# Kernel tuning notes

Hardware: AMD Instinct MI355X
Metric: run time of the kernel (lower is better)

The kernel has to match this reference:

```python
import jax, jax.numpy as jnp
import numpy as np

B, S, D, H = 4, 2048, 1024, 16
DK = D // H


def setup_inputs() -> dict:
    key = jax.random.key(0)
    ks = jax.random.split(key, 9)
    sc = 1.0 / np.sqrt(D)
    return {
        "query": jax.random.normal(ks[0], (B, S, D), jnp.float32),
        "key": jax.random.normal(ks[1], (B, S, D), jnp.float32),
        "value": jax.random.normal(ks[2], (B, S, D), jnp.float32),
        "Wq": jax.random.normal(ks[3], (D, D), jnp.float32) * sc,
        "bq": jax.random.normal(ks[4], (D,), jnp.float32) * sc,
        "Wk": jax.random.normal(ks[5], (D, D), jnp.float32) * sc,
        "bk": jax.random.normal(ks[6], (D,), jnp.float32) * sc,
        "Wv": jax.random.normal(ks[7], (D, D), jnp.float32) * sc,
        "bv": jax.random.normal(ks[8], (D,), jnp.float32) * sc,
    }


def reference(query, key, value, Wq, bq, Wk, bk, Wv, bv):
    # QKV projections, split into heads: [B,S,D] -> [B,H,S,DK]
    q = (query @ Wq + bq).reshape(B, S, H, DK).transpose(0, 2, 1, 3)
    k = (key @ Wk + bk).reshape(B, S, H, DK).transpose(0, 2, 1, 3)
    v = (value @ Wv + bv).reshape(B, S, H, DK).transpose(0, 2, 1, 3)
    # NOTE: original module applies NO 1/sqrt(d_k) scaling
    attn = jnp.einsum("bhqd,bhkd->bhqk", q, k)
    attn = jax.nn.softmax(attn, axis=-1)  # dropout is identity at inference
    ctx = jnp.einsum("bhqk,bhkd->bhqd", attn, v)
    ctx = ctx.transpose(0, 2, 1, 3).reshape(B, S, D)
    # original adds residual to raw concatenated context (no output projection)
    return ctx + query
```

## Files before the change

kernel.cpp:

```cpp
#include <hip/hip_runtime.h>
#include <hip/hip_bf16.h>
#include <stdint.h>

#define Bb 4
#define Ss 2048
#define Dd 1024
#define Hh 16
#define DK 64
#define BH 64
#define Mm 8192
#define KVT 64

typedef __attribute__((ext_vector_type(8))) _Float16 f16x8;
typedef __attribute__((ext_vector_type(4))) _Float16 f16x4;
typedef __attribute__((ext_vector_type(2))) __fp16 fp16x2;
typedef __attribute__((ext_vector_type(4))) float f32x4;
typedef __attribute__((ext_vector_type(16))) float f32x16;
typedef __attribute__((ext_vector_type(2))) unsigned uint2v;

__device__ __forceinline__ void gload16(const _Float16* g, _Float16* lds) {
  __builtin_amdgcn_global_load_lds((const __attribute__((address_space(1))) unsigned int*)g,
                                   (__attribute__((address_space(3))) unsigned int*)lds, 16, 0, 0);
}

#if __has_builtin(__builtin_amdgcn_exp2f)
__device__ __forceinline__ float ex2(float x) { return __builtin_amdgcn_exp2f(x); }
#else
__device__ __forceinline__ float ex2(float x) {
  float r; asm("v_exp_f32 %0, %1" : "=v"(r) : "v"(x)); return r;
}
#endif

__device__ __forceinline__ unsigned pk2u(float a, float b) {
  union { fp16x2 h; unsigned u; } x;
  x.h = __builtin_amdgcn_cvt_pkrtz(a, b);
  return x.u;
}

__global__ __launch_bounds__(256) void cvt_act(const float* __restrict__ q,
                                               const float* __restrict__ k,
                                               const float* __restrict__ v,
                                               _Float16* __restrict__ xq,
                                               _Float16* __restrict__ xk,
                                               _Float16* __restrict__ xv) {
  const float* src = blockIdx.z == 0 ? q : (blockIdx.z == 1 ? k : v);
  _Float16* dst = blockIdx.z == 0 ? xq : (blockIdx.z == 1 ? xk : xv);
  int i = (blockIdx.x * 256 + threadIdx.x) * 8;
  float4 a = *(const float4*)(src + i);
  float4 b = *(const float4*)(src + i + 4);
  union { f16x8 v8; _Float16 h[8]; } o;
  o.h[0] = (_Float16)a.x; o.h[1] = (_Float16)a.y; o.h[2] = (_Float16)a.z; o.h[3] = (_Float16)a.w;
  o.h[4] = (_Float16)b.x; o.h[5] = (_Float16)b.y; o.h[6] = (_Float16)b.z; o.h[7] = (_Float16)b.w;
  *(f16x8*)(dst + i) = o.v8;
}

__global__ __launch_bounds__(256) void cvt_wt(const float* __restrict__ wq,
                                              const float* __restrict__ wk,
                                              const float* __restrict__ wv,
                                              _Float16* __restrict__ tq,
                                              _Float16* __restrict__ tk,
                                              _Float16* __restrict__ tv) {
  const float* w = blockIdx.z == 0 ? wq : (blockIdx.z == 1 ? wk : wv);
  _Float16* o = blockIdx.z == 0 ? tq : (blockIdx.z == 1 ? tk : tv);
  float wscale = blockIdx.z == 0 ? 1.4426950408889634f : 1.0f;
  __shared__ float tile[64][65];
  int k0 = blockIdx.x * 64;
  int n0 = blockIdx.y * 64;
  int t = threadIdx.x;
  int tr = t >> 4;
  int tc = (t & 15) * 4;
  for (int i = 0; i < 4; i++) {
    int r = i * 16 + tr;
    float4 val = *(const float4*)(w + (k0 + r) * Dd + n0 + tc);
    tile[r][tc + 0] = val.x; tile[r][tc + 1] = val.y;
    tile[r][tc + 2] = val.z; tile[r][tc + 3] = val.w;
  }
  __syncthreads();
  for (int i = 0; i < 2; i++) {
    int vdx = t + 256 * i;
    int rn = vdx >> 3;
    int c8 = (vdx & 7) * 8;
    union { f16x8 v8; _Float16 h[8]; } o2;
    for (int j = 0; j < 8; j++) o2.h[j] = (_Float16)(tile[c8 + j][rn] * wscale);
    *(f16x8*)(o + (n0 + rn) * Dd + k0 + c8) = o2.v8;
  }
}

__global__ __launch_bounds__(256) void gemm_qkv(
    const _Float16* __restrict__ xq, const _Float16* __restrict__ xk,
    const _Float16* __restrict__ xv,
    const _Float16* __restrict__ wtq, const _Float16* __restrict__ wtk,
    const _Float16* __restrict__ wtv,
    const float* __restrict__ bq, const float* __restrict__ bk, const float* __restrict__ bv,
    _Float16* __restrict__ oq, _Float16* __restrict__ ok,
    _Float16* __restrict__ ov) {
  int z = blockIdx.z;
  const _Float16* A  = z == 0 ? xq  : (z == 1 ? xk  : xv);
  const _Float16* Bt = z == 0 ? wtq : (z == 1 ? wtk : wtv);
  const float* bias  = z == 0 ? bq  : (z == 1 ? bk  : bv);
  _Float16* out      = z == 0 ? oq  : (z == 1 ? ok  : ov);
  float bscale       = z == 0 ? 1.4426950408889634f : 1.0f;

  __shared__ _Float16 As[128 * 64];
  __shared__ _Float16 Bs[128 * 64];

  int tid = threadIdx.x;
  int w = tid >> 6;
  int l = tid & 63;
  int lr = l & 15, lk = l >> 4;
  int m0 = blockIdx.x * 128;
  int n0 = blockIdx.y * 128;
  int wr = (w >> 1) * 64;
  int wc = (w & 1) * 64;

  f32x4 acc[4][4] = {};

  for (int kt = 0; kt < Dd; kt += 64) {
    __syncthreads();
    for (int i = 0; i < 4; i++) {
      int fbase = i * 256 + w * 64;
      int f = fbase + l;
      int r = f >> 3, c = (f & 7) * 8;
      gload16(A + (m0 + r) * Dd + kt + c, &As[fbase * 8]);
      gload16(Bt + (n0 + r) * Dd + kt + c, &Bs[fbase * 8]);
    }
    __syncthreads();
    for (int kh = 0; kh < 2; kh++) {
      f16x8 af[4], bfr[4];
      for (int mi = 0; mi < 4; mi++)
        af[mi] = *(const f16x8*)&As[(wr + mi * 16 + lr) * 64 + kh * 32 + lk * 8];
      for (int ni = 0; ni < 4; ni++)
        bfr[ni] = *(const f16x8*)&Bs[(wc + ni * 16 + lr) * 64 + kh * 32 + lk * 8];
      for (int mi = 0; mi < 4; mi++)
        for (int ni = 0; ni < 4; ni++)
          acc[mi][ni] = __builtin_amdgcn_mfma_f32_16x16x32_f16(af[mi], bfr[ni], acc[mi][ni], 0, 0, 0);
    }
  }

  if (z == 2) {
    for (int mi = 0; mi < 4; mi++) {
      for (int ni = 0; ni < 4; ni++) {
        int n = n0 + wc + ni * 16 + lr;
        float bval = bias[n];
        int h = n >> 6, dk = n & 63;
        int m = m0 + wr + mi * 16 + lk * 4;
        int b = m >> 11, s = m & 2047;
        f16x4 o4;
        for (int j = 0; j < 4; j++) o4[j] = (_Float16)(acc[mi][ni][j] + bval);
        *(f16x4*)(out + ((size_t)((b * Hh + h) * DK + dk) * Ss + s)) = o4;
      }
    }
  } else {
    for (int mi = 0; mi < 4; mi++) {
      for (int ni = 0; ni < 4; ni++) {
        int n = n0 + wc + ni * 16 + lr;
        float bval = bias[n] * bscale;
        int h = n >> 6, dk = n & 63;
        for (int j = 0; j < 4; j++) {
          int m = m0 + wr + mi * 16 + lk * 4 + j;
          int b = m >> 11, s = m & 2047;
          out[((b * Hh + h) * Ss + s) * DK + dk] = (_Float16)(acc[mi][ni][j] + bval);
        }
      }
    }
  }
}

__global__ __launch_bounds__(256) void attn(const _Float16* __restrict__ Qb,
                                            const _Float16* __restrict__ Kb,
                                            const _Float16* __restrict__ Vt,
                                            const float* __restrict__ query,
                                            float* __restrict__ outp) {
  __shared__ _Float16 Kl[2][KVT * 64];
  __shared__ _Float16 Vl[2][KVT * 64];

  int tid = threadIdx.x;
  int w = tid >> 6, l = tid & 63;
  int l31 = l & 31, hi = l >> 5;
  int bh = blockIdx.x;
  int q0 = blockIdx.y * 128 + w * 32;
  const _Float16* Qp = Qb + bh * (Ss * DK);
  const _Float16* Kp = Kb + bh * (Ss * DK);
  const _Float16* Vp = Vt + bh * (DK * Ss);

  int srow = l >> 3;
  int sslot = (l & 7) ^ (srow & 7);
  int w16 = w * 16;
  const _Float16* ksrc0 = Kp + (w16 + srow) * DK + sslot * 8;
  const _Float16* ksrc1 = Kp + (w16 + 8 + srow) * DK + sslot * 8;
  const _Float16* vsrc0 = Vp + (w16 + srow) * Ss + sslot * 8;
  const _Float16* vsrc1 = Vp + (w16 + 8 + srow) * Ss + sslot * 8;

#define STAGE(KV0, BUF)                                                   \
  {                                                                       \
    gload16(ksrc0 + (KV0) * DK, &Kl[BUF][w16 * 64]);                      \
    gload16(ksrc1 + (KV0) * DK, &Kl[BUF][(w16 + 8) * 64]);                \
    gload16(vsrc0 + (KV0), &Vl[BUF][w16 * 64]);                           \
    gload16(vsrc1 + (KV0), &Vl[BUF][(w16 + 8) * 64]);                     \
  }

  f16x8 qf[4];
#pragma unroll
  for (int s = 0; s < 4; s++)
    qf[s] = *(const f16x8*)(Qp + (q0 + l31) * DK + s * 16 + hi * 8);

  f32x16 o0 = {}, o1 = {};
  float mrun = -1e30f, lrun = 0.f;

  int kv7 = l31 & 7;
  int rslot[4];
#pragma unroll
  for (int s = 0; s < 4; s++) rslot[s] = ((s * 2 + hi) ^ kv7) * 8;

  STAGE(0, 0)
  __syncthreads();

  int cur = 0;
  for (int kv0 = 0; kv0 < Ss; kv0 += KVT) {
    if (kv0 + KVT < Ss) STAGE(kv0 + KVT, cur ^ 1)

    const _Float16* Kc = &Kl[cur][0];
    f32x16 s0 = {}, s1 = {};
#pragma unroll
    for (int s = 0; s < 4; s++) {
      f16x8 ka = *(const f16x8*)&Kc[l31 * 64 + rslot[s]];
      s0 = __builtin_amdgcn_mfma_f32_32x32x16_f16(ka, qf[s], s0, 0, 0, 0);
    }
#pragma unroll
    for (int s = 0; s < 4; s++) {
      f16x8 kb = *(const f16x8*)&Kc[(32 + l31) * 64 + rslot[s]];
      s1 = __builtin_amdgcn_mfma_f32_32x32x16_f16(kb, qf[s], s1, 0, 0, 0);
    }

    float m8[8];
#pragma unroll
    for (int r = 0; r < 8; r++)
      m8[r] = fmaxf(fmaxf(s0[r], s0[r + 8]), fmaxf(s1[r], s1[r + 8]));
#pragma unroll
    for (int d = 4; d >= 1; d >>= 1)
#pragma unroll
      for (int r = 0; r < 4; r++) if (r < d) m8[r] = fmaxf(m8[r], m8[r + d]);
    float pm = fmaxf(m8[0], __shfl_xor(m8[0], 32));

    if (!__all(pm - mrun <= 8.f)) {
      float mn = fmaxf(mrun, pm);
      float sc_ = ex2(mrun - mn);
      mrun = mn;
      lrun *= sc_;
#pragma unroll
      for (int r = 0; r < 16; r++) { o0[r] *= sc_; o1[r] *= sc_; }
    }
#pragma unroll
    for (int r = 0; r < 16; r++) {
      s0[r] = ex2(s0[r] - mrun);
      s1[r] = ex2(s1[r] - mrun);
    }
    float s8[8];
#pragma unroll
    for (int r = 0; r < 8; r++) s8[r] = (s0[r] + s0[r + 8]) + (s1[r] + s1[r + 8]);
#pragma unroll
    for (int d = 4; d >= 1; d >>= 1)
#pragma unroll
      for (int r = 0; r < 4; r++) if (r < d) s8[r] += s8[r + d];
    lrun += s8[0];

    const _Float16* Vc = &Vl[cur][0];
#define PVSTEP(SRC, OFF, KST)                                                   \
    {                                                                           \
      unsigned a0 = pk2u(SRC[(OFF) + 0], SRC[(OFF) + 1]);                       \
      unsigned a1 = pk2u(SRC[(OFF) + 2], SRC[(OFF) + 3]);                       \
      unsigned b0 = pk2u(SRC[(OFF) + 4], SRC[(OFF) + 5]);                       \
      unsigned b1 = pk2u(SRC[(OFF) + 6], SRC[(OFF) + 7]);                       \
      uint2v r0 = __builtin_amdgcn_permlane32_swap(a0, b0, false, false);       \
      uint2v r1 = __builtin_amdgcn_permlane32_swap(a1, b1, false, false);       \
      union { unsigned u[4]; f16x8 v; } pf;                                     \
      pf.u[0] = r0[0]; pf.u[1] = r1[0]; pf.u[2] = r0[1]; pf.u[3] = r1[1];       \
      f16x8 v0 = *(const f16x8*)&Vc[l31 * 64 + rslot[KST]];                     \
      f16x8 v1 = *(const f16x8*)&Vc[(32 + l31) * 64 + rslot[KST]];              \
      o0 = __builtin_amdgcn_mfma_f32_32x32x16_f16(v0, pf.v, o0, 0, 0, 0);       \
      o1 = __builtin_amdgcn_mfma_f32_32x32x16_f16(v1, pf.v, o1, 0, 0, 0);       \
    }
    PVSTEP(s0, 0, 0)
    PVSTEP(s0, 8, 1)
    PVSTEP(s1, 0, 2)
    PVSTEP(s1, 8, 3)
#undef PVSTEP

    __syncthreads();
    cur ^= 1;
  }

  lrun += __shfl_xor(lrun, 32);
  int b = bh >> 4, h = bh & 15;
  float inv = 1.f / lrun;
  int base = (b * Ss + q0 + l31) * Dd + h * 64;
#pragma unroll
  for (int rq = 0; rq < 4; rq++) {
    int d0 = rq * 8 + hi * 4;
    float4 qv0 = *(const float4*)(query + base + d0);
    float4 ov0;
    ov0.x = o0[rq * 4 + 0] * inv + qv0.x;
    ov0.y = o0[rq * 4 + 1] * inv + qv0.y;
    ov0.z = o0[rq * 4 + 2] * inv + qv0.z;
    ov0.w = o0[rq * 4 + 3] * inv + qv0.w;
    *(float4*)(outp + base + d0) = ov0;
    float4 qv1 = *(const float4*)(query + base + 32 + d0);
    float4 ov1;
    ov1.x = o1[rq * 4 + 0] * inv + qv1.x;
    ov1.y = o1[rq * 4 + 1] * inv + qv1.y;
    ov1.z = o1[rq * 4 + 2] * inv + qv1.z;
    ov1.w = o1[rq * 4 + 3] * inv + qv1.w;
    *(float4*)(outp + base + 32 + d0) = ov1;
  }
#undef STAGE
}

extern "C" void kernel_launch(void* const* d_in, const int* in_sizes, int n_in,
                              void* d_out, int out_size, void* d_ws, size_t ws_size,
                              hipStream_t stream) {
  const float* query = (const float*)d_in[0];
  const float* key   = (const float*)d_in[1];
  const float* value = (const float*)d_in[2];
  const float* Wq = (const float*)d_in[3];
  const float* bq = (const float*)d_in[4];
  const float* Wk = (const float*)d_in[5];
  const float* bk = (const float*)d_in[6];
  const float* Wv = (const float*)d_in[7];
  const float* bv = (const float*)d_in[8];
  float* out = (float*)d_out;

  _Float16* ws = (_Float16*)d_ws;
  const size_t ACT = (size_t)Mm * Dd;
  const size_t WSZ = (size_t)Dd * Dd;
  _Float16* Xq   = ws;
  _Float16* Xk   = Xq + ACT;
  _Float16* Xv   = Xk + ACT;
  _Float16* Wtq  = Xv + ACT;
  _Float16* Wtk  = Wtq + WSZ;
  _Float16* Wtv  = Wtk + WSZ;
  _Float16* Qb   = Wtv + WSZ;
  _Float16* Kb   = Qb + ACT;
  _Float16* VtT  = Kb + ACT;

  cvt_act<<<dim3(4096, 1, 3), dim3(256), 0, stream>>>(query, key, value, Xq, Xk, Xv);
  cvt_wt<<<dim3(16, 16, 3), dim3(256), 0, stream>>>(Wq, Wk, Wv, Wtq, Wtk, Wtv);
  gemm_qkv<<<dim3(64, 8, 3), dim3(256), 0, stream>>>(Xq, Xk, Xv, Wtq, Wtk, Wtv,
                                                     bq, bk, bv, Qb, Kb, VtT);
  attn<<<dim3(64, 16), dim3(256), 0, stream>>>(Qb, Kb, VtT, query, out);
}
```

Measured before the change: 221.2 us.

## Process 64 query rows per wave and compute row sums via MFMA

Each wave now handles two 32-row query tiles against the same K/V shared-memory tiles, doubling reuse of each LDS load and halving the grid to 512 blocks. The per-row softmax denominator is no longer reduced with scalar adds; it is accumulated by an extra MFMA against a ones vector alongside the PV product. This raises register pressure (four output accumulators plus two sum accumulators) and halves block count, which may reduce occupancy on a 256-CU device.

```diff
diff --git a/kernel.cpp b/kernel.cpp
--- a/kernel.cpp
+++ b/kernel.cpp
@@ -178,7 +178,7 @@
   int w = tid >> 6, l = tid & 63;
   int l31 = l & 31, hi = l >> 5;
   int bh = blockIdx.x;
-  int q0 = blockIdx.y * 128 + w * 32;
+  int q0 = blockIdx.y * 256 + w * 64;
   const _Float16* Qp = Qb + bh * (Ss * DK);
   const _Float16* Kp = Kb + bh * (Ss * DK);
   const _Float16* Vp = Vt + bh * (DK * Ss);
@@ -199,13 +199,20 @@
     gload16(vsrc1 + (KV0), &Vl[BUF][(w16 + 8) * 64]);                     \
   }
 
-  f16x8 qf[4];
+  f16x8 qfA[4], qfB[4];
 #pragma unroll
-  for (int s = 0; s < 4; s++)
-    qf[s] = *(const f16x8*)(Qp + (q0 + l31) * DK + s * 16 + hi * 8);
-
-  f32x16 o0 = {}, o1 = {};
-  float mrun = -1e30f, lrun = 0.f;
+  for (int s = 0; s < 4; s++) {
+    qfA[s] = *(const f16x8*)(Qp + (q0 + l31) * DK + s * 16 + hi * 8);
+    qfB[s] = *(const f16x8*)(Qp + (q0 + 32 + l31) * DK + s * 16 + hi * 8);
+  }
+
+  f16x8 ones;
+#pragma unroll
+  for (int j = 0; j < 8; j++) ones[j] = (_Float16)1.0f;
+
+  f32x16 oA0 = {}, oA1 = {}, oB0 = {}, oB1 = {};
+  f32x16 smA = {}, smB = {};
+  float mrunA = -1e30f, mrunB = -1e30f;
 
   int kv7 = l31 & 7;
   int rslot[4];
@@ -220,98 +227,111 @@
     if (kv0 + KVT < Ss) STAGE(kv0 + KVT, cur ^ 1)
 
     const _Float16* Kc = &Kl[cur][0];
-    f32x16 s0 = {}, s1 = {};
+    f32x16 sA0 = {}, sA1 = {}, sB0 = {}, sB1 = {};
 #pragma unroll
     for (int s = 0; s < 4; s++) {
       f16x8 ka = *(const f16x8*)&Kc[l31 * 64 + rslot[s]];
-      s0 = __builtin_amdgcn_mfma_f32_32x32x16_f16(ka, qf[s], s0, 0, 0, 0);
-    }
-#pragma unroll
-    for (int s = 0; s < 4; s++) {
       f16x8 kb = *(const f16x8*)&Kc[(32 + l31) * 64 + rslot[s]];
-      s1 = __builtin_amdgcn_mfma_f32_32x32x16_f16(kb, qf[s], s1, 0, 0, 0);
-    }
-
-    float m8[8];
-#pragma unroll
-    for (int r = 0; r < 8; r++)
-      m8[r] = fmaxf(fmaxf(s0[r], s0[r + 8]), fmaxf(s1[r], s1[r + 8]));
-#pragma unroll
-    for (int d = 4; d >= 1; d >>= 1)
-#pragma unroll
-      for (int r = 0; r < 4; r++) if (r < d) m8[r] = fmaxf(m8[r], m8[r + d]);
-    float pm = fmaxf(m8[0], __shfl_xor(m8[0], 32));
-
-    if (!__all(pm - mrun <= 8.f)) {
-      float mn = fmaxf(mrun, pm);
-      float sc_ = ex2(mrun - mn);
-      mrun = mn;
-      lrun *= sc_;
-#pragma unroll
-      for (int r = 0; r < 16; r++) { o0[r] *= sc_; o1[r] *= sc_; }
-    }
-#pragma unroll
-    for (int r = 0; r < 16; r++) {
-      s0[r] = ex2(s0[r] - mrun);
-      s1[r] = ex2(s1[r] - mrun);
-    }
-    float s8[8];
-#pragma unroll
-    for (int r = 0; r < 8; r++) s8[r] = (s0[r] + s0[r + 8]) + (s1[r] + s1[r + 8]);
-#pragma unroll
-    for (int d = 4; d >= 1; d >>= 1)
-#pragma unroll
-      for (int r = 0; r < 4; r++) if (r < d) s8[r] += s8[r + d];
-    lrun += s8[0];
+      sA0 = __builtin_amdgcn_mfma_f32_32x32x16_f16(ka, qfA[s], sA0, 0, 0, 0);
+      sA1 = __builtin_amdgcn_mfma_f32_32x32x16_f16(kb, qfA[s], sA1, 0, 0, 0);
+      sB0 = __builtin_amdgcn_mfma_f32_32x32x16_f16(ka, qfB[s], sB0, 0, 0, 0);
+      sB1 = __builtin_amdgcn_mfma_f32_32x32x16_f16(kb, qfB[s], sB1, 0, 0, 0);
+    }
+
+#define SOFTMAX(S0, S1, MRUN, O0, O1, SM)                                       \
+    {                                                                           \
+      float m8[8];                                                              \
+      _Pragma("unroll")                                                         \
+      for (int r = 0; r < 8; r++)                                               \
+        m8[r] = fmaxf(fmaxf(S0[r], S0[r + 8]), fmaxf(S1[r], S1[r + 8]));        \
+      _Pragma("unroll")                                                         \
+      for (int d = 4; d >= 1; d >>= 1)                                          \
+        for (int r = 0; r < 4; r++) if (r < d) m8[r] = fmaxf(m8[r], m8[r + d]); \
+      float pm = fmaxf(m8[0], __shfl_xor(m8[0], 32));                           \
+      if (!__all(pm - MRUN <= 8.f)) {                                           \
+        float mn = fmaxf(MRUN, pm);                                             \
+        float sc_ = ex2(MRUN - mn);                                             \
+        MRUN = mn;                                                              \
+        _Pragma("unroll")                                                       \
+        for (int r = 0; r < 16; r++) {                                          \
+          O0[r] *= sc_; O1[r] *= sc_; SM[r] *= sc_;                             \
+        }                                                                       \
+      }                                                                         \
+      _Pragma("unroll")                                                         \
+      for (int r = 0; r < 16; r++) {                                            \
+        S0[r] = ex2(S0[r] - MRUN);                                              \
+        S1[r] = ex2(S1[r] - MRUN);                                              \
+      }                                                                         \
+    }
+    SOFTMAX(sA0, sA1, mrunA, oA0, oA1, smA)
+    SOFTMAX(sB0, sB1, mrunB, oB0, oB1, smB)
+#undef SOFTMAX
 
     const _Float16* Vc = &Vl[cur][0];
-#define PVSTEP(SRC, OFF, KST)                                                   \
+#define PVSTEP(SA, SB, OFF, KST)                                                \
     {                                                                           \
-      unsigned a0 = pk2u(SRC[(OFF) + 0], SRC[(OFF) + 1]);                       \
-      unsigned a1 = pk2u(SRC[(OFF) + 2], SRC[(OFF) + 3]);                       \
-      unsigned b0 = pk2u(SRC[(OFF) + 4], SRC[(OFF) + 5]);                       \
-      unsigned b1 = pk2u(SRC[(OFF) + 6], SRC[(OFF) + 7]);                       \
-      uint2v r0 = __builtin_amdgcn_permlane32_swap(a0, b0, false, false);       \
-      uint2v r1 = __builtin_amdgcn_permlane32_swap(a1, b1, false, false);       \
-      union { unsigned u[4]; f16x8 v; } pf;                                     \
-      pf.u[0] = r0[0]; pf.u[1] = r1[0]; pf.u[2] = r0[1]; pf.u[3] = r1[1];       \
       f16x8 v0 = *(const f16x8*)&Vc[l31 * 64 + rslot[KST]];                     \
       f16x8 v1 = *(const f16x8*)&Vc[(32 + l31) * 64 + rslot[KST]];              \
-      o0 = __builtin_amdgcn_mfma_f32_32x32x16_f16(v0, pf.v, o0, 0, 0, 0);       \
-      o1 = __builtin_amdgcn_mfma_f32_32x32x16_f16(v1, pf.v, o1, 0, 0, 0);       \
-    }
-    PVSTEP(s0, 0, 0)
-    PVSTEP(s0, 8, 1)
-    PVSTEP(s1, 0, 2)
-    PVSTEP(s1, 8, 3)
+      unsigned aa0 = pk2u(SA[(OFF) + 0], SA[(OFF) + 1]);                        \
+      unsigned aa1 = pk2u(SA[(OFF) + 2], SA[(OFF) + 3]);                        \
+      unsigned ab0 = pk2u(SA[(OFF) + 4], SA[(OFF) + 5]);                        \
+      unsigned ab1 = pk2u(SA[(OFF) + 6], SA[(OFF) + 7]);                        \
+      uint2v ra0 = __builtin_amdgcn_permlane32_swap(aa0, ab0, false, false);    \
+      uint2v ra1 = __builtin_amdgcn_permlane32_swap(aa1, ab1, false, false);    \
+      union { unsigned u[4]; f16x8 v; } pfA;                                    \
+      pfA.u[0] = ra0[0]; pfA.u[1] = ra1[0]; pfA.u[2] = ra0[1]; pfA.u[3] = ra1[1];\
+      unsigned ba0 = pk2u(SB[(OFF) + 0], SB[(OFF) + 1]);                        \
+      unsigned ba1 = pk2u(SB[(OFF) + 2], SB[(OFF) + 3]);                        \
+      unsigned bb0 = pk2u(SB[(OFF) + 4], SB[(OFF) + 5]);                        \
+      unsigned bb1 = pk2u(SB[(OFF) + 6], SB[(OFF) + 7]);                        \
+      uint2v rb0 = __builtin_amdgcn_permlane32_swap(ba0, bb0, false, false);    \
+      uint2v rb1 = __builtin_amdgcn_permlane32_swap(ba1, bb1, false, false);    \
+      union { unsigned u[4]; f16x8 v; } pfB;                                    \
+      pfB.u[0] = rb0[0]; pfB.u[1] = rb1[0]; pfB.u[2] = rb0[1]; pfB.u[3] = rb1[1];\
+      oA0 = __builtin_amdgcn_mfma_f32_32x32x16_f16(v0, pfA.v, oA0, 0, 0, 0);    \
+      oA1 = __builtin_amdgcn_mfma_f32_32x32x16_f16(v1, pfA.v, oA1, 0, 0, 0);    \
+      oB0 = __builtin_amdgcn_mfma_f32_32x32x16_f16(v0, pfB.v, oB0, 0, 0, 0);    \
+      oB1 = __builtin_amdgcn_mfma_f32_32x32x16_f16(v1, pfB.v, oB1, 0, 0, 0);    \
+      smA = __builtin_amdgcn_mfma_f32_32x32x16_f16(ones, pfA.v, smA, 0, 0, 0);  \
+      smB = __builtin_amdgcn_mfma_f32_32x32x16_f16(ones, pfB.v, smB, 0, 0, 0);  \
+    }
+    PVSTEP(sA0, sB0, 0, 0)
+    PVSTEP(sA0, sB0, 8, 1)
+    PVSTEP(sA1, sB1, 0, 2)
+    PVSTEP(sA1, sB1, 8, 3)
 #undef PVSTEP
 
     __syncthreads();
     cur ^= 1;
   }
 
-  lrun += __shfl_xor(lrun, 32);
   int b = bh >> 4, h = bh & 15;
-  float inv = 1.f / lrun;
-  int base = (b * Ss + q0 + l31) * Dd + h * 64;
-#pragma unroll
-  for (int rq = 0; rq < 4; rq++) {
-    int d0 = rq * 8 + hi * 4;
-    float4 qv0 = *(const float4*)(query + base + d0);
-    float4 ov0;
-    ov0.x = o0[rq * 4 + 0] * inv + qv0.x;
-    ov0.y = o0[rq * 4 + 1] * inv + qv0.y;
-    ov0.z = o0[rq * 4 + 2] * inv + qv0.z;
-    ov0.w = o0[rq * 4 + 3] * inv + qv0.w;
-    *(float4*)(outp + base + d0) = ov0;
-    float4 qv1 = *(const float4*)(query + base + 32 + d0);
-    float4 ov1;
-    ov1.x = o1[rq * 4 + 0] * inv + qv1.x;
-    ov1.y = o1[rq * 4 + 1] * inv + qv1.y;
-    ov1.z = o1[rq * 4 + 2] * inv + qv1.z;
-    ov1.w = o1[rq * 4 + 3] * inv + qv1.w;
-    *(float4*)(outp + base + 32 + d0) = ov1;
-  }
+#define WRITEOUT(O0, O1, SM, QOFF)                                              \
+  {                                                                             \
+    float inv = 1.f / SM[0];                                                    \
+    int base = (b * Ss + q0 + (QOFF) + l31) * Dd + h * 64;                      \
+    _Pragma("unroll")                                                           \
+    for (int rq = 0; rq < 4; rq++) {                                            \
+      int d0 = rq * 8 + hi * 4;                                                 \
+      float4 qv0 = *(const float4*)(query + base + d0);                         \
+      float4 ov0;                                                               \
+      ov0.x = O0[rq * 4 + 0] * inv + qv0.x;                                     \
+      ov0.y = O0[rq * 4 + 1] * inv + qv0.y;                                     \
+      ov0.z = O0[rq * 4 + 2] * inv + qv0.z;                                     \
+      ov0.w = O0[rq * 4 + 3] * inv + qv0.w;                                     \
+      *(float4*)(outp + base + d0) = ov0;                                       \
+      float4 qv1 = *(const float4*)(query + base + 32 + d0);                    \
+      float4 ov1;                                                               \
+      ov1.x = O1[rq * 4 + 0] * inv + qv1.x;                                     \
+      ov1.y = O1[rq * 4 + 1] * inv + qv1.y;                                     \
+      ov1.z = O1[rq * 4 + 2] * inv + qv1.z;                                     \
+      ov1.w = O1[rq * 4 + 3] * inv + qv1.w;                                     \
+      *(float4*)(outp + base + 32 + d0) = ov1;                                  \
+    }                                                                           \
+  }
+  WRITEOUT(oA0, oA1, smA, 0)
+  WRITEOUT(oB0, oB1, smB, 32)
+#undef WRITEOUT
 #undef STAGE
 }
 
@@ -346,5 +366,5 @@
   cvt_wt<<<dim3(16, 16, 3), dim3(256), 0, stream>>>(Wq, Wk, Wv, Wtq, Wtk, Wtv);
   gemm_qkv<<<dim3(64, 8, 3), dim3(256), 0, stream>>>(Xq, Xk, Xv, Wtq, Wtk, Wtv,
                                                      bq, bk, bv, Qb, Kb, VtT);
-  attn<<<dim3(64, 16), dim3(256), 0, stream>>>(Qb, Kb, VtT, query, out);
-}
+  attn<<<dim3(64, 8), dim3(256), 0, stream>>>(Qb, Kb, VtT, query, out);
+}
```

Result: slower. 252.3 us (+14.1%).
